# Optimization experiments

Measured on AMD Instinct MI355X. Metric: run time of the kernel, lower is better.

The kernel has to match this reference:

```python
import jax, jax.numpy as jnp
import numpy as np

N = 50000   # nodes
E = 800000  # directed edges (avg degree 16)
IN = 128    # input feature dim
H = 4       # heads in conv1
C = 64      # per-head hidden dim
NEG_SLOPE = 0.2  # PyG GATConv leaky_relu slope


def setup_inputs() -> dict:
    key = jax.random.key(0)
    ks = jax.random.split(key, 10)
    def glorot(k, shape):
        fan = shape[0] + shape[-1]
        return jax.random.normal(k, shape, jnp.float32) * np.sqrt(2.0 / fan)
    return {
        "x": jax.random.normal(ks[0], (N, IN), jnp.float32),
        "edge_index": jax.random.randint(ks[1], (2, E), 0, N, jnp.int32),
        "W1": glorot(ks[2], (IN, H * C)),
        "att_src1": glorot(ks[3], (H, C)),
        "att_dst1": glorot(ks[4], (H, C)),
        "b1": jnp.zeros((H * C,), jnp.float32),
        "W2": glorot(ks[5], (H * C, C)),
        "att_src2": glorot(ks[6], (1, C)),
        "att_dst2": glorot(ks[7], (1, C)),
        "b2": jnp.zeros((C,), jnp.float32),
    }


def _gat_layer(x, src, dst, W, att_src, att_dst, bias, concat):
    # x: [N, F_in]; W: [F_in, H*C]; att_*: [H, C]
    n = x.shape[0]
    h, c = att_src.shape
    hx = (x @ W).reshape(n, h, c)                      # [N, H, C]
    a_s = jnp.einsum('nhc,hc->nh', hx, att_src)        # per-node source score
    a_d = jnp.einsum('nhc,hc->nh', hx, att_dst)        # per-node target score
    e = jax.nn.leaky_relu(a_s[src] + a_d[dst], NEG_SLOPE)   # [Etot, H]
    # segment softmax over edges grouped by destination node
    m = jax.ops.segment_max(e, dst, num_segments=n)
    p = jnp.exp(e - m[dst])
    s = jax.ops.segment_sum(p, dst, num_segments=n)
    alpha = p / (s[dst] + 1e-16)                       # [Etot, H]
    out = jax.ops.segment_sum(hx[src] * alpha[:, :, None], dst, num_segments=n)
    out = out.reshape(n, h * c) if concat else out.mean(axis=1)
    return out + bias


def reference(x, edge_index, W1, att_src1, att_dst1, b1, W2, att_src2, att_dst2, b2):
    n = x.shape[0]
    loops = jnp.arange(n, dtype=edge_index.dtype)      # PyG add_self_loops=True
    src = jnp.concatenate([edge_index[0], loops])
    dst = jnp.concatenate([edge_index[1], loops])
    h1 = jax.nn.elu(_gat_layer(x, src, dst, W1, att_src1, att_dst1, b1, True))
    return _gat_layer(h1, src, dst, W2, att_src2, att_dst2, b2, False)
```

## Files before the change

### kernel.cpp

```cpp
#include <hip/hip_runtime.h>
#include <hip/hip_bf16.h>
#include <hip/hip_fp16.h>

using f16x8 = __attribute__((ext_vector_type(8))) _Float16;
using f32x4 = __attribute__((ext_vector_type(4))) float;

__device__ __forceinline__ float leaky(float x){ return (x >= 0.f) ? x : 0.2f * x; }

__global__ __launch_bounds__(256) void f32_to_f16(const float* __restrict__ in,
                                                  __half* __restrict__ out, size_t n4){
  size_t i = (size_t)blockIdx.x * 256 + threadIdx.x;
  size_t stride = (size_t)gridDim.x * 256;
  for (; i < n4; i += stride){
    float4 v = ((const float4*)in)[i];
    __half2 a = __floats2half2_rn(v.x, v.y);
    __half2 b = __floats2half2_rn(v.z, v.w);
    uint2 u = make_uint2(*(unsigned*)&a, *(unsigned*)&b);
    *(uint2*)(out + i * 4) = u;
  }
}

__global__ __launch_bounds__(256) void pack_W(const float* __restrict__ W,
                                              __half* __restrict__ Wf, int K, int N){
  int t = blockIdx.x * 256 + threadIdx.x;
  if (t >= K * N) return;
  int j    = t & 7;
  int lane = (t >> 3) & 63;
  int rest = t >> 9;
  int nt16 = N >> 4;
  int ntg  = rest % nt16;
  int ksg  = rest / nt16;
  int k = ksg * 32 + ((lane >> 4) << 3) + j;
  int n = ntg * 16 + (lane & 15);
  Wf[t] = __float2half_rn(W[(size_t)k * N + n]);
}

__global__ __launch_bounds__(256) void gemm_mfma(const __half* __restrict__ A,
                                                 const __half* __restrict__ Wf,
                                                 __half* __restrict__ C,
                                                 const float* __restrict__ att_s_w,
                                                 const float* __restrict__ att_d_w,
                                                 float* __restrict__ a_s_out,
                                                 float* __restrict__ a_d_out,
                                                 int M, int N, int K, int H){
  __shared__ __half As[64 * 64];
  const int tid  = threadIdx.x;
  const int l    = tid & 63;
  const int w    = tid >> 6;
  const int brow = blockIdx.x * 64;
  const int bcol = blockIdx.y * 64;
  const int NT16 = N >> 4;
  const int cl   = l & 15;
  const int kg   = l >> 4;
  const int arow = w * 16 + cl;

  f32x4 acc[4] = {};

  for (int kb = 0; kb < K; kb += 64){
    #pragma unroll
    for (int s = tid; s < 512; s += 256){
      int r  = s >> 3;
      int c8 = (s & 7) << 3;
      uint4 v = make_uint4(0u, 0u, 0u, 0u);
      if (brow + r < M) v = *(const uint4*)(A + (size_t)(brow + r) * K + kb + c8);
      *(uint4*)&As[r * 64 + (c8 ^ ((r & 7) << 3))] = v;
    }
    __syncthreads();
    #pragma unroll
    for (int ks = 0; ks < 2; ++ks){
      int ckk = ks * 32 + kg * 8;
      f16x8 af = *(const f16x8*)&As[arow * 64 + (ckk ^ ((arow & 7) << 3))];
      int ksg = (kb >> 5) + ks;
      const __half* wbase = Wf + ((size_t)(ksg * NT16 + (bcol >> 4)) * 64 + l) * 8;
      #pragma unroll
      for (int nt = 0; nt < 4; ++nt){
        f16x8 bf = *(const f16x8*)(wbase + (size_t)nt * 512);
        acc[nt] = __builtin_amdgcn_mfma_f32_16x16x32_f16(af, bf, acc[nt], 0, 0, 0);
      }
    }
    __syncthreads();
  }

  const int head = bcol >> 6;
  float aws[4], awd[4];
  #pragma unroll
  for (int nt = 0; nt < 4; ++nt){
    aws[nt] = att_s_w[bcol + nt * 16 + cl];
    awd[nt] = att_d_w[bcol + nt * 16 + cl];
  }
  #pragma unroll
  for (int i = 0; i < 4; ++i){
    int row = brow + w * 16 + kg * 4 + i;
    bool ok = row < M;
    float s = 0.f, dd = 0.f;
    #pragma unroll
    for (int nt = 0; nt < 4; ++nt){
      float c = acc[nt][i];
      if (ok) C[(size_t)row * N + bcol + nt * 16 + cl] = __float2half_rn(c);
      s  = fmaf(c, aws[nt], s);
      dd = fmaf(c, awd[nt], dd);
    }
    #pragma unroll
    for (int m = 1; m < 16; m <<= 1){
      s  += __shfl_xor(s,  m, 64);
      dd += __shfl_xor(dd, m, 64);
    }
    if (ok && cl == 0){
      a_s_out[(size_t)row * H + head] = s;
      a_d_out[(size_t)row * H + head] = dd;
    }
  }
}

__global__ __launch_bounds__(256) void build_deg(const int* __restrict__ ei,
                                                 int E, int N, int* __restrict__ deg){
  int e = blockIdx.x * blockDim.x + threadIdx.x;
  if (e >= E + N) return;
  int dst = (e < E) ? ei[E + e] : (e - E);
  atomicAdd(&deg[dst], 1);
}

__global__ __launch_bounds__(1024) void scan_phase1(const int* __restrict__ deg,
                                                    int* __restrict__ rowptr,
                                                    int* __restrict__ bsum, int n){
  __shared__ int buf[1024];
  int tid = threadIdx.x;
  int i = blockIdx.x * 1024 + tid;
  int v = (i < n) ? deg[i] : 0;
  buf[tid] = v;
  __syncthreads();
  #pragma unroll
  for (int off = 1; off < 1024; off <<= 1){
    int t = (tid >= off) ? buf[tid - off] : 0;
    __syncthreads();
    buf[tid] += t;
    __syncthreads();
  }
  if (i < n) rowptr[i] = buf[tid] - v;
  if (tid == 1023) bsum[blockIdx.x] = buf[1023];
}

__global__ __launch_bounds__(64) void scan_phase2(const int* __restrict__ bsum,
                                                  int* __restrict__ boff,
                                                  int* __restrict__ rowptr,
                                                  int nb, int n){
  int lane = threadIdx.x;
  int v = (lane < nb) ? bsum[lane] : 0;
  int orig = v;
  #pragma unroll
  for (int off = 1; off < 64; off <<= 1){
    int t = __shfl_up(v, off, 64);
    if (lane >= off) v += t;
  }
  if (lane < nb) boff[lane] = v - orig;
  if (lane == nb - 1) rowptr[n] = v;
}

__global__ __launch_bounds__(1024) void scan_phase3(int* __restrict__ rowptr,
                                                    int* __restrict__ pos,
                                                    const int* __restrict__ boff, int n){
  int i = blockIdx.x * 1024 + threadIdx.x;
  if (i >= n) return;
  int val = rowptr[i] + boff[blockIdx.x];
  rowptr[i] = val;
  pos[i] = val;
}

__global__ __launch_bounds__(256) void build_csr(const int* __restrict__ ei,
                                                 int E, int N,
                                                 int* __restrict__ pos,
                                                 int* __restrict__ csr_src){
  int e = blockIdx.x * blockDim.x + threadIdx.x;
  if (e >= E + N) return;
  int src, dst;
  if (e < E){ src = ei[e]; dst = ei[E + e]; }
  else      { src = dst = e - E; }
  int slot = atomicAdd(&pos[dst], 1);
  csr_src[slot] = src;
}

__global__ __launch_bounds__(256) void fused_agg1(const int* __restrict__ rowptr,
                                                  const int* __restrict__ csr,
                                                  const float* __restrict__ a_s,
                                                  const float* __restrict__ a_d,
                                                  const __half* __restrict__ hx,
                                                  const float* __restrict__ bias,
                                                  __half* __restrict__ h1, int n){
  int d = blockIdx.x * 4 + (threadIdx.x >> 6);
  if (d >= n) return;
  int l = threadIdx.x & 63;
  int h_ = l >> 4;
  int beg = __builtin_amdgcn_readfirstlane(rowptr[d]);
  int end = __builtin_amdgcn_readfirstlane(rowptr[d + 1]);
  float adh = a_d[d * 4 + h_];

  float4 acc = make_float4(0.f, 0.f, 0.f, 0.f);
  float sum = 0.f;

  float e0, e1; uint2 r0, r1;
  {
    int s0 = csr[beg];
    e0 = a_s[s0 * 4 + h_];
    r0 = *((const uint2*)(hx + (size_t)s0 * 256) + l);
  }
  const bool two = (beg + 1 < end);
  if (two){
    int s1 = csr[beg + 1];
    e1 = a_s[s1 * 4 + h_];
    r1 = *((const uint2*)(hx + (size_t)s1 * 256) + l);
  }
  for (int j = beg + 2; j < end; ++j){
    int s2 = csr[j];
    float e2 = a_s[s2 * 4 + h_];
    uint2 r2 = *((const uint2*)(hx + (size_t)s2 * 256) + l);
    float p = __expf(leaky(e0 + adh));
    sum += p;
    float2 f0 = __half22float2(*(__half2*)&r0.x);
    float2 f1 = __half22float2(*(__half2*)&r0.y);
    acc.x = fmaf(p, f0.x, acc.x); acc.y = fmaf(p, f0.y, acc.y);
    acc.z = fmaf(p, f1.x, acc.z); acc.w = fmaf(p, f1.y, acc.w);
    e0 = e1; r0 = r1;
    e1 = e2; r1 = r2;
  }
  {
    float p = __expf(leaky(e0 + adh));
    sum += p;
    float2 f0 = __half22float2(*(__half2*)&r0.x);
    float2 f1 = __half22float2(*(__half2*)&r0.y);
    acc.x = fmaf(p, f0.x, acc.x); acc.y = fmaf(p, f0.y, acc.y);
    acc.z = fmaf(p, f1.x, acc.z); acc.w = fmaf(p, f1.y, acc.w);
  }
  if (two){
    float p = __expf(leaky(e1 + adh));
    sum += p;
    float2 f0 = __half22float2(*(__half2*)&r1.x);
    float2 f1 = __half22float2(*(__half2*)&r1.y);
    acc.x = fmaf(p, f0.x, acc.x); acc.y = fmaf(p, f0.y, acc.y);
    acc.z = fmaf(p, f1.x, acc.z); acc.w = fmaf(p, f1.y, acc.w);
  }

  float inv = 1.f / (sum + 1e-16f);
  float4 b4 = *(const float4*)(bias + (l << 2));
  float4 o;
  o.x = acc.x * inv + b4.x; o.y = acc.y * inv + b4.y;
  o.z = acc.z * inv + b4.z; o.w = acc.w * inv + b4.w;
  o.x = (o.x > 0.f) ? o.x : (__expf(o.x) - 1.f);
  o.y = (o.y > 0.f) ? o.y : (__expf(o.y) - 1.f);
  o.z = (o.z > 0.f) ? o.z : (__expf(o.z) - 1.f);
  o.w = (o.w > 0.f) ? o.w : (__expf(o.w) - 1.f);
  __half2 u0 = __floats2half2_rn(o.x, o.y);
  __half2 u1 = __floats2half2_rn(o.z, o.w);
  uint2 uu = make_uint2(*(unsigned*)&u0, *(unsigned*)&u1);
  *(uint2*)(h1 + (size_t)d * 256 + (l << 2)) = uu;
}

__global__ __launch_bounds__(256) void fused_agg2(const int* __restrict__ rowptr,
                                                  const int* __restrict__ csr,
                                                  const float* __restrict__ a_s,
                                                  const float* __restrict__ a_d,
                                                  const __half* __restrict__ hx,
                                                  const float* __restrict__ bias,
                                                  float* __restrict__ out, int n){
  int d = blockIdx.x * 4 + (threadIdx.x >> 6);
  if (d >= n) return;
  int l = threadIdx.x & 63;
  int beg = __builtin_amdgcn_readfirstlane(rowptr[d]);
  int end = __builtin_amdgcn_readfirstlane(rowptr[d + 1]);
  float ad = a_d[d];

  float acc = 0.f, sum = 0.f;
  float e0, e1; __half r0, r1;
  {
    int s0 = csr[beg];
    e0 = a_s[s0];
    r0 = hx[(size_t)s0 * 64 + l];
  }
  const bool two = (beg + 1 < end);
  if (two){
    int s1 = csr[beg + 1];
    e1 = a_s[s1];
    r1 = hx[(size_t)s1 * 64 + l];
  }
  for (int j = beg + 2; j < end; ++j){
    int s2 = csr[j];
    float e2 = a_s[s2];
    __half r2 = hx[(size_t)s2 * 64 + l];
    float p = __expf(leaky(e0 + ad));
    sum += p;
    acc = fmaf(p, __half2float(r0), acc);
    e0 = e1; r0 = r1;
    e1 = e2; r1 = r2;
  }
  {
    float p = __expf(leaky(e0 + ad));
    sum += p;
    acc = fmaf(p, __half2float(r0), acc);
  }
  if (two){
    float p = __expf(leaky(e1 + ad));
    sum += p;
    acc = fmaf(p, __half2float(r1), acc);
  }
  out[(size_t)d * 64 + l] = acc / (sum + 1e-16f) + bias[l];
}

extern "C" void kernel_launch(void* const* d_in, const int* in_sizes, int n_in,
                              void* d_out, int out_size, void* d_ws, size_t ws_size,
                              hipStream_t stream){
  const float* x        = (const float*)d_in[0];
  const int*   ei       = (const int*)  d_in[1];
  const float* W1       = (const float*)d_in[2];
  const float* att_src1 = (const float*)d_in[3];
  const float* att_dst1 = (const float*)d_in[4];
  const float* b1       = (const float*)d_in[5];
  const float* W2       = (const float*)d_in[6];
  const float* att_src2 = (const float*)d_in[7];
  const float* att_dst2 = (const float*)d_in[8];
  const float* b2       = (const float*)d_in[9];
  float* out = (float*)d_out;

  const int IN = 128, HC = 256, C = 64;
  const int N  = in_sizes[0] / IN;
  const int E  = in_sizes[1] / 2;
  const int ET = E + N;
  const int NB = (N + 1023) / 1024;

  char* ws = (char*)d_ws;
  size_t off = 0;
  auto carve = [&](size_t bytes) -> char* {
    off = (off + 255) & ~(size_t)255;
    char* p = ws + off;
    off += bytes;
    return p;
  };
  __half* xh    = (__half*)carve((size_t)N * IN * 2);
  __half* W1f   = (__half*)carve((size_t)IN * HC * 2);
  __half* W2f   = (__half*)carve((size_t)HC * C * 2);
  __half* hx1h  = (__half*)carve((size_t)N * HC * 2);
  __half* h1h   = (__half*)carve((size_t)N * HC * 2);
  __half* hx2h  = (__half*)carve((size_t)N * C * 2);
  float*  as1   = (float*) carve((size_t)N * 4 * 4);
  float*  ad1   = (float*) carve((size_t)N * 4 * 4);
  float*  as2   = (float*) carve((size_t)N * 4);
  float*  ad2   = (float*) carve((size_t)N * 4);
  int*    deg   = (int*)   carve((size_t)N * 4);
  int*    rowptr= (int*)   carve((size_t)(N + 1) * 4);
  int*    pos   = (int*)   carve((size_t)N * 4);
  int*    csr   = (int*)   carve((size_t)ET * 4);
  int*    bsum  = (int*)   carve(64 * 4);
  int*    boff  = (int*)   carve(64 * 4);

  f32_to_f16<<<2048, 256, 0, stream>>>(x, xh, (size_t)N * IN / 4);
  pack_W<<<(IN * HC + 255) / 256, 256, 0, stream>>>(W1, W1f, IN, HC);
  pack_W<<<(HC * C + 255) / 256, 256, 0, stream>>>(W2, W2f, HC, C);

  hipMemsetAsync(deg, 0, (size_t)N * 4, stream);
  build_deg<<<(ET + 255) / 256, 256, 0, stream>>>(ei, E, N, deg);
  scan_phase1<<<NB, 1024, 0, stream>>>(deg, rowptr, bsum, N);
  scan_phase2<<<1, 64, 0, stream>>>(bsum, boff, rowptr, NB, N);
  scan_phase3<<<NB, 1024, 0, stream>>>(rowptr, pos, boff, N);
  build_csr<<<(ET + 255) / 256, 256, 0, stream>>>(ei, E, N, pos, csr);

  dim3 g1((N + 63) / 64, HC / 64);
  gemm_mfma<<<g1, 256, 0, stream>>>(xh, W1f, hx1h, att_src1, att_dst1,
                                    as1, ad1, N, HC, IN, 4);
  fused_agg1<<<(N + 3) / 4, 256, 0, stream>>>(rowptr, csr, as1, ad1, hx1h, b1, h1h, N);

  dim3 g2((N + 63) / 64, C / 64);
  gemm_mfma<<<g2, 256, 0, stream>>>(h1h, W2f, hx2h, att_src2, att_dst2,
                                    as2, ad2, N, C, HC, 1);
  fused_agg2<<<(N + 3) / 4, 256, 0, stream>>>(rowptr, csr, as2, ad2, hx2h, b2, out, N);
}
```

Baseline: 339.0 us.

## Fuse prep kernels, merge scan phases, and batch-prefetch edges in aggregation

Merges the x conversion, both weight packs and the degree memset into one prep kernel, and folds the block-offset scan into scan_phase3, which removes several launches. Both aggregation kernels switch from a two-deep rolling prefetch to double-buffered batches of four edges, so more gathers are in flight per wave. Padding lanes reload the first neighbour and are masked with p=0. This adds redundant loads and predication on low-degree nodes, and uses more registers.

```diff
diff --git a/kernel.cpp b/kernel.cpp
--- a/kernel.cpp
+++ b/kernel.cpp
@@ -7,23 +7,9 @@
 
 __device__ __forceinline__ float leaky(float x){ return (x >= 0.f) ? x : 0.2f * x; }
 
-__global__ __launch_bounds__(256) void f32_to_f16(const float* __restrict__ in,
-                                                  __half* __restrict__ out, size_t n4){
-  size_t i = (size_t)blockIdx.x * 256 + threadIdx.x;
-  size_t stride = (size_t)gridDim.x * 256;
-  for (; i < n4; i += stride){
-    float4 v = ((const float4*)in)[i];
-    __half2 a = __floats2half2_rn(v.x, v.y);
-    __half2 b = __floats2half2_rn(v.z, v.w);
-    uint2 u = make_uint2(*(unsigned*)&a, *(unsigned*)&b);
-    *(uint2*)(out + i * 4) = u;
-  }
-}
-
-__global__ __launch_bounds__(256) void pack_W(const float* __restrict__ W,
-                                              __half* __restrict__ Wf, int K, int N){
-  int t = blockIdx.x * 256 + threadIdx.x;
-  if (t >= K * N) return;
+__device__ __forceinline__ void pack_w_elem(const float* __restrict__ W,
+                                            __half* __restrict__ Wf,
+                                            int t, int N){
   int j    = t & 7;
   int lane = (t >> 3) & 63;
   int rest = t >> 9;
@@ -33,6 +19,27 @@
   int k = ksg * 32 + ((lane >> 4) << 3) + j;
   int n = ntg * 16 + (lane & 15);
   Wf[t] = __float2half_rn(W[(size_t)k * N + n]);
+}
+
+__global__ __launch_bounds__(256) void prep_kernel(const float* __restrict__ x,
+                                                   __half* __restrict__ xh, size_t n4,
+                                                   const float* __restrict__ W1,
+                                                   __half* __restrict__ W1f, int kn1, int n1,
+                                                   const float* __restrict__ W2,
+                                                   __half* __restrict__ W2f, int kn2, int n2,
+                                                   int* __restrict__ deg, int N){
+  size_t gid = (size_t)blockIdx.x * 256 + threadIdx.x;
+  size_t stride = (size_t)gridDim.x * 256;
+  for (size_t i = gid; i < n4; i += stride){
+    float4 v = ((const float4*)x)[i];
+    __half2 a = __floats2half2_rn(v.x, v.y);
+    __half2 b = __floats2half2_rn(v.z, v.w);
+    uint2 u = make_uint2(*(unsigned*)&a, *(unsigned*)&b);
+    *(uint2*)(xh + i * 4) = u;
+  }
+  for (size_t t = gid; t < (size_t)kn1; t += stride) pack_w_elem(W1, W1f, (int)t, n1);
+  for (size_t t = gid; t < (size_t)kn2; t += stride) pack_w_elem(W2, W2f, (int)t, n2);
+  for (size_t i = gid; i < (size_t)N; i += stride) deg[i] = 0;
 }
 
 __global__ __launch_bounds__(256) void gemm_mfma(const __half* __restrict__ A,
@@ -140,28 +147,29 @@
   if (tid == 1023) bsum[blockIdx.x] = buf[1023];
 }
 
-__global__ __launch_bounds__(64) void scan_phase2(const int* __restrict__ bsum,
-                                                  int* __restrict__ boff,
-                                                  int* __restrict__ rowptr,
-                                                  int nb, int n){
-  int lane = threadIdx.x;
-  int v = (lane < nb) ? bsum[lane] : 0;
-  int orig = v;
-  #pragma unroll
-  for (int off = 1; off < 64; off <<= 1){
-    int t = __shfl_up(v, off, 64);
-    if (lane >= off) v += t;
-  }
-  if (lane < nb) boff[lane] = v - orig;
-  if (lane == nb - 1) rowptr[n] = v;
-}
-
 __global__ __launch_bounds__(1024) void scan_phase3(int* __restrict__ rowptr,
                                                     int* __restrict__ pos,
-                                                    const int* __restrict__ boff, int n){
-  int i = blockIdx.x * 1024 + threadIdx.x;
+                                                    const int* __restrict__ bsum,
+                                                    int nb, int n){
+  __shared__ int s_off;
+  __shared__ int s_tot;
+  int tid = threadIdx.x;
+  if (tid < 64){
+    int v = (tid < nb) ? bsum[tid] : 0;
+    int orig = v;
+    #pragma unroll
+    for (int off = 1; off < 64; off <<= 1){
+      int t = __shfl_up(v, off, 64);
+      if (tid >= off) v += t;
+    }
+    if (tid == (int)blockIdx.x) s_off = v - orig;
+    if (tid == nb - 1) s_tot = v;
+  }
+  __syncthreads();
+  if (blockIdx.x == 0 && tid == 0) rowptr[n] = s_tot;
+  int i = blockIdx.x * 1024 + tid;
   if (i >= n) return;
-  int val = rowptr[i] + boff[blockIdx.x];
+  int val = rowptr[i] + s_off;
   rowptr[i] = val;
   pos[i] = val;
 }
@@ -197,46 +205,40 @@
   float4 acc = make_float4(0.f, 0.f, 0.f, 0.f);
   float sum = 0.f;
 
-  float e0, e1; uint2 r0, r1;
-  {
-    int s0 = csr[beg];
-    e0 = a_s[s0 * 4 + h_];
-    r0 = *((const uint2*)(hx + (size_t)s0 * 256) + l);
-  }
-  const bool two = (beg + 1 < end);
-  if (two){
-    int s1 = csr[beg + 1];
-    e1 = a_s[s1 * 4 + h_];
-    r1 = *((const uint2*)(hx + (size_t)s1 * 256) + l);
-  }
-  for (int j = beg + 2; j < end; ++j){
-    int s2 = csr[j];
-    float e2 = a_s[s2 * 4 + h_];
-    uint2 r2 = *((const uint2*)(hx + (size_t)s2 * 256) + l);
-    float p = __expf(leaky(e0 + adh));
-    sum += p;
-    float2 f0 = __half22float2(*(__half2*)&r0.x);
-    float2 f1 = __half22float2(*(__half2*)&r0.y);
-    acc.x = fmaf(p, f0.x, acc.x); acc.y = fmaf(p, f0.y, acc.y);
-    acc.z = fmaf(p, f1.x, acc.z); acc.w = fmaf(p, f1.y, acc.w);
-    e0 = e1; r0 = r1;
-    e1 = e2; r1 = r2;
-  }
-  {
-    float p = __expf(leaky(e0 + adh));
-    sum += p;
-    float2 f0 = __half22float2(*(__half2*)&r0.x);
-    float2 f1 = __half22float2(*(__half2*)&r0.y);
-    acc.x = fmaf(p, f0.x, acc.x); acc.y = fmaf(p, f0.y, acc.y);
-    acc.z = fmaf(p, f1.x, acc.z); acc.w = fmaf(p, f1.y, acc.w);
-  }
-  if (two){
-    float p = __expf(leaky(e1 + adh));
-    sum += p;
-    float2 f0 = __half22float2(*(__half2*)&r1.x);
-    float2 f1 = __half22float2(*(__half2*)&r1.y);
-    acc.x = fmaf(p, f0.x, acc.x); acc.y = fmaf(p, f0.y, acc.y);
-    acc.z = fmaf(p, f1.x, acc.z); acc.w = fmaf(p, f1.y, acc.w);
+  auto LOAD = [&](int j0, float (&e)[4], uint2 (&r)[4]){
+    #pragma unroll
+    for (int t = 0; t < 4; ++t){
+      int j = j0 + t;
+      int s = (j < end) ? csr[j] : csr[beg];
+      e[t] = a_s[s * 4 + h_];
+      r[t] = *((const uint2*)(hx + (size_t)s * 256) + l);
+    }
+  };
+  auto CONS = [&](int j0, float (&e)[4], uint2 (&r)[4]){
+    #pragma unroll
+    for (int t = 0; t < 4; ++t){
+      bool in = (j0 + t < end);
+      float p = in ? __expf(leaky(e[t] + adh)) : 0.f;
+      sum += p;
+      float2 f0 = __half22float2(*(__half2*)&r[t].x);
+      float2 f1 = __half22float2(*(__half2*)&r[t].y);
+      acc.x = fmaf(p, f0.x, acc.x); acc.y = fmaf(p, f0.y, acc.y);
+      acc.z = fmaf(p, f1.x, acc.z); acc.w = fmaf(p, f1.y, acc.w);
+    }
+  };
+
+  float eA[4], eB[4]; uint2 rA[4], rB[4];
+  int j0 = beg;
+  LOAD(j0, eA, rA);
+  while (true){
+    int j1 = j0 + 4;
+    if (j1 < end) LOAD(j1, eB, rB);
+    CONS(j0, eA, rA);
+    j0 = j1; if (j0 >= end) break;
+    j1 = j0 + 4;
+    if (j1 < end) LOAD(j1, eA, rA);
+    CONS(j0, eB, rB);
+    j0 = j1; if (j0 >= end) break;
   }
 
   float inv = 1.f / (sum + 1e-16f);
@@ -269,38 +271,40 @@
   float ad = a_d[d];
 
   float acc = 0.f, sum = 0.f;
-  float e0, e1; __half r0, r1;
-  {
-    int s0 = csr[beg];
-    e0 = a_s[s0];
-    r0 = hx[(size_t)s0 * 64 + l];
-  }
-  const bool two = (beg + 1 < end);
-  if (two){
-    int s1 = csr[beg + 1];
-    e1 = a_s[s1];
-    r1 = hx[(size_t)s1 * 64 + l];
-  }
-  for (int j = beg + 2; j < end; ++j){
-    int s2 = csr[j];
-    float e2 = a_s[s2];
-    __half r2 = hx[(size_t)s2 * 64 + l];
-    float p = __expf(leaky(e0 + ad));
-    sum += p;
-    acc = fmaf(p, __half2float(r0), acc);
-    e0 = e1; r0 = r1;
-    e1 = e2; r1 = r2;
-  }
-  {
-    float p = __expf(leaky(e0 + ad));
-    sum += p;
-    acc = fmaf(p, __half2float(r0), acc);
-  }
-  if (two){
-    float p = __expf(leaky(e1 + ad));
-    sum += p;
-    acc = fmaf(p, __half2float(r1), acc);
-  }
+
+  auto LOAD = [&](int j0, float (&e)[4], unsigned short (&r)[4]){
+    #pragma unroll
+    for (int t = 0; t < 4; ++t){
+      int j = j0 + t;
+      int s = (j < end) ? csr[j] : csr[beg];
+      e[t] = a_s[s];
+      r[t] = *(const unsigned short*)(hx + (size_t)s * 64 + l);
+    }
+  };
+  auto CONS = [&](int j0, float (&e)[4], unsigned short (&r)[4]){
+    #pragma unroll
+    for (int t = 0; t < 4; ++t){
+      bool in = (j0 + t < end);
+      float p = in ? __expf(leaky(e[t] + ad)) : 0.f;
+      sum += p;
+      acc = fmaf(p, __half2float(*(__half*)&r[t]), acc);
+    }
+  };
+
+  float eA[4], eB[4]; unsigned short rA[4], rB[4];
+  int j0 = beg;
+  LOAD(j0, eA, rA);
+  while (true){
+    int j1 = j0 + 4;
+    if (j1 < end) LOAD(j1, eB, rB);
+    CONS(j0, eA, rA);
+    j0 = j1; if (j0 >= end) break;
+    j1 = j0 + 4;
+    if (j1 < end) LOAD(j1, eA, rA);
+    CONS(j0, eB, rB);
+    j0 = j1; if (j0 >= end) break;
+  }
+
   out[(size_t)d * 64 + l] = acc / (sum + 1e-16f) + bias[l];
 }
 
@@ -348,17 +352,15 @@
   int*    pos   = (int*)   carve((size_t)N * 4);
   int*    csr   = (int*)   carve((size_t)ET * 4);
   int*    bsum  = (int*)   carve(64 * 4);
-  int*    boff  = (int*)   carve(64 * 4);
-
-  f32_to_f16<<<2048, 256, 0, stream>>>(x, xh, (size_t)N * IN / 4);
-  pack_W<<<(IN * HC + 255) / 256, 256, 0, stream>>>(W1, W1f, IN, HC);
-  pack_W<<<(HC * C + 255) / 256, 256, 0, stream>>>(W2, W2f, HC, C);
-
-  hipMemsetAsync(deg, 0, (size_t)N * 4, stream);
+
+  prep_kernel<<<2048, 256, 0, stream>>>(x, xh, (size_t)N * IN / 4,
+                                        W1, W1f, IN * HC, HC,
+                                        W2, W2f, HC * C, C,
+                                        deg, N);
+
   build_deg<<<(ET + 255) / 256, 256, 0, stream>>>(ei, E, N, deg);
   scan_phase1<<<NB, 1024, 0, stream>>>(deg, rowptr, bsum, N);
-  scan_phase2<<<1, 64, 0, stream>>>(bsum, boff, rowptr, NB, N);
-  scan_phase3<<<NB, 1024, 0, stream>>>(rowptr, pos, boff, N);
+  scan_phase3<<<NB, 1024, 0, stream>>>(rowptr, pos, bsum, NB, N);
   build_csr<<<(ET + 255) / 256, 256, 0, stream>>>(ei, E, N, pos, csr);
 
   dim3 g1((N + 63) / 64, HC / 64);
```

Measured after the change: 318.6 us. 6.0% less time.
